# Performance work log

Measured on AMD Instinct MI355X. Metric: run time of the kernel, lower is better.

Reference implementation:

```python
import jax, jax.numpy as jnp
import numpy as np

N, OBS_LEN, PRED_LEN = 8192, 20, 30
EMBED, HIDDEN, CNN_OUT = 64, 128, 2048


def setup_inputs() -> dict:
    key = jax.random.key(0)
    ks = jax.random.split(key, 13)
    s = 0.05
    return {
        "img_embedding": jax.random.normal(ks[0], (N, CNN_OUT), jnp.float32),
        "obs_pos": jax.random.normal(ks[1], (N, OBS_LEN, 2), jnp.float32),
        "obs_hist_size": jax.random.randint(ks[2], (N,), 0, 20, jnp.int64) if jax.config.jax_enable_x64 else jax.random.randint(ks[2], (N,), 0, 20, jnp.int32),
        "obs_pos_rel": jax.random.normal(ks[3], (N, OBS_LEN, 2), jnp.float32),
        "h0": jax.random.normal(ks[4], (1, HIDDEN), jnp.float32) * s,
        "W_ih": jax.random.normal(ks[5], (4 * HIDDEN, EMBED), jnp.float32) * s,
        "W_hh": jax.random.normal(ks[6], (4 * HIDDEN, HIDDEN), jnp.float32) * s,
        "b_ih": jax.random.normal(ks[7], (4 * HIDDEN,), jnp.float32) * s,
        "b_hh": jax.random.normal(ks[8], (4 * HIDDEN,), jnp.float32) * s,
        "embed_W": jax.random.normal(ks[9], (EMBED, 2), jnp.float32) * s,
        "embed_b": jax.random.normal(ks[10], (EMBED,), jnp.float32) * s,
        "pred_W": jax.random.normal(ks[11], (2, HIDDEN + CNN_OUT), jnp.float32) * s,
        "pred_b": jax.random.normal(ks[12], (2,), jnp.float32) * s,
    }


def reference(img_embedding, obs_pos, obs_hist_size, obs_pos_rel,
              h0, W_ih, W_hh, b_ih, b_hh, embed_W, embed_b, pred_W, pred_b):
    n, obs_len = obs_pos.shape[0], obs_pos.shape[1]

    def lstm_cell(x_emb, h, c):
        # torch gate order: i, f, g, o
        gates = x_emb @ W_ih.T + b_ih + h @ W_hh.T + b_hh  # [n, 4H]
        i, f, g, o = jnp.split(gates, 4, axis=-1)
        c2 = jax.nn.sigmoid(f) * c + jax.nn.sigmoid(i) * jnp.tanh(g)
        h2 = jax.nn.sigmoid(o) * jnp.tanh(c2)
        return h2, c2

    def embed(rel):
        return jax.nn.relu(rel @ embed_W.T + embed_b)

    # NOTE: original code initializes BOTH h and c from h0 (faithful to source).
    h = jnp.broadcast_to(h0, (n, h0.shape[1]))
    c = h

    # ---- observation phase: t = 1 .. obs_len-1, masked update ----
    def obs_step(carry, inp):
        h, c = carry
        rel_t, t = inp
        mask = (obs_hist_size > (obs_len - t))[:, None]  # [n, 1]
        h2, c2 = lstm_cell(embed(rel_t), h, c)
        h = jnp.where(mask, h2, h)
        c = jnp.where(mask, c2, c)
        return (h, c), None

    ts = jnp.arange(1, obs_len)
    rel_seq = jnp.swapaxes(obs_pos_rel[:, 1:, :], 0, 1)  # [obs_len-1, n, 2]
    (h, c), _ = jax.lax.scan(obs_step, (h, c), (rel_seq, ts))

    def pred_step(carry, _):
        h, c, pos = carry
        disp = jnp.concatenate([h, img_embedding], axis=1) @ pred_W.T + pred_b  # [n, 2]
        pos = pos + disp
        h, c = lstm_cell(embed(disp), h, c)
        return (h, c, pos), pos

    pos0 = obs_pos[:, -1, :]
    _, traj = jax.lax.scan(pred_step, (h, c, pos0), None, length=PRED_LEN)
    return jnp.swapaxes(traj, 0, 1)  # [n, pred_len, 2]
```

## Files before the change

kernel.cpp:

```cpp
#include <hip/hip_runtime.h>

#define OBS_LEN 20
#define PRED_LEN 30
#define MBLK 32

typedef __attribute__((ext_vector_type(8))) short bf16x8;
typedef __attribute__((ext_vector_type(4))) float f32x4;

__device__ __forceinline__ unsigned short f2bf(float x){
  unsigned int u = __float_as_uint(x);
  u = u + 0x7FFFu + ((u >> 16) & 1u);
  return (unsigned short)(u >> 16);
}

__device__ __forceinline__ float sigm(float x){
  return __builtin_amdgcn_rcpf(1.0f + __expf(-x));
}
__device__ __forceinline__ float tanh_(float x){
  return 1.0f - 2.0f*__builtin_amdgcn_rcpf(__expf(2.0f*x) + 1.0f);
}

__global__ __launch_bounds__(512, 2) void traj_kernel(
    const float* __restrict__ img, const float* __restrict__ obs_pos,
    const int* __restrict__ hist, const float* __restrict__ rel,
    const float* __restrict__ h0, const float* __restrict__ W_ih,
    const float* __restrict__ W_hh, const float* __restrict__ b_ih,
    const float* __restrict__ b_hh, const float* __restrict__ eW,
    const float* __restrict__ eb, const float* __restrict__ pW,
    const float* __restrict__ pb, float* __restrict__ out)
{
  __shared__ unsigned short xh[MBLK*200];
  __shared__ float hf[MBLK*132];
  __shared__ float relL[MBLK*40];
  __shared__ float pwL[2*128];
  __shared__ float eW0[64], eW1[64], ebL[64];
  __shared__ float dispL[MBLK*2];
  __shared__ float imgcL[MBLK*2];

  const int tid  = threadIdx.x;
  const int wv   = tid >> 6;
  const int lane = tid & 63;
  const int q    = lane >> 4;
  const int i    = lane & 15;
  const int j    = wv*16 + i;
  const int g0   = blockIdx.x * MBLK;

  for (int idx = tid; idx < MBLK*40; idx += 512) relL[idx] = rel[g0*40 + idx];
  if (tid < 256) pwL[tid] = pW[(tid >> 7)*2176 + (tid & 127)];
  if (tid < 64){ eW0[tid] = eW[tid*2]; eW1[tid] = eW[tid*2+1]; ebL[tid] = eb[tid]; }

  {
    int m = tid >> 4, i16 = tid & 15;
    const float* row = img + (size_t)(g0 + m)*2048 + i16*128;
    const float* p0  = pW + 128 + i16*128;
    const float* p1  = pW + 2176 + 128 + i16*128;
    float s0 = 0.f, s1 = 0.f;
    #pragma unroll
    for (int v = 0; v < 32; v++){
      float4 a  = ((const float4*)row)[v];
      float4 w0 = ((const float4*)p0)[v];
      float4 w1 = ((const float4*)p1)[v];
      s0 += a.x*w0.x + a.y*w0.y + a.z*w0.z + a.w*w0.w;
      s1 += a.x*w1.x + a.y*w1.y + a.z*w1.z + a.w*w1.w;
    }
    #pragma unroll
    for (int msk = 1; msk < 16; msk <<= 1){
      s0 += __shfl_xor(s0, msk);
      s1 += __shfl_xor(s1, msk);
    }
    if (i16 == 0){ imgcL[m*2] = s0; imgcL[m*2+1] = s1; }
  }

  float h0j = h0[j];
  float bias_s[4];
  #pragma unroll
  for (int nt = 0; nt < 4; nt++) bias_s[nt] = b_ih[nt*128 + j] + b_hh[nt*128 + j];

  int   hist_s[8];
  float c_s[8], h_s[8];
  #pragma unroll
  for (int mt = 0; mt < 2; mt++)
    #pragma unroll
    for (int r = 0; r < 4; r++){
      int m = mt*16 + q*4 + r;
      hist_s[mt*4+r] = hist[g0 + m];
      c_s[mt*4+r] = h0j; h_s[mt*4+r] = h0j;
      xh[m*200 + 64 + j] = f2bf(h0j);
      hf[m*132 + j] = h0j;
    }

  bf16x8 Bf[4][6];
  #pragma unroll
  for (int nt = 0; nt < 4; nt++){
    int row = nt*128 + j;
    #pragma unroll
    for (int kt = 0; kt < 6; kt++){
      const float* src = (kt < 2) ? (W_ih + row*64  + kt*32      + q*8)
                                  : (W_hh + row*128 + (kt-2)*32  + q*8);
      float4 lo = ((const float4*)src)[0];
      float4 hi = ((const float4*)src)[1];
      bf16x8 tf;
      tf[0]=(short)f2bf(lo.x); tf[1]=(short)f2bf(lo.y); tf[2]=(short)f2bf(lo.z); tf[3]=(short)f2bf(lo.w);
      tf[4]=(short)f2bf(hi.x); tf[5]=(short)f2bf(hi.y); tf[6]=(short)f2bf(hi.z); tf[7]=(short)f2bf(hi.w);
      Bf[nt][kt] = tf;
    }
  }

  const int dm  = tid >> 4;
  const int dod = (tid >> 3) & 1;
  float pos_r = obs_pos[(size_t)(g0 + dm)*40 + 38 + dod];
  float pb_r  = pb[dod];
  size_t out_base = (size_t)(g0 + dm)*60 + dod;

  __syncthreads();
  float imgc_r = imgcL[dm*2 + dod];

  f32x4 acc[2][4];

  for (int step = 0; step < 49; step++){
    const bool obs = (step < 19);
    const int  t   = step + 1;
    if (!obs){
      __syncthreads();
      int i8 = tid & 7;
      const float* hrow = &hf[dm*132 + i8*16];
      const float* prow = &pwL[dod*128 + i8*16];
      float s = 0.f;
      #pragma unroll
      for (int v = 0; v < 4; v++){
        float4 h4 = ((const float4*)hrow)[v];
        float4 p4 = ((const float4*)prow)[v];
        s += h4.x*p4.x + h4.y*p4.y + h4.z*p4.z + h4.w*p4.w;
      }
      s += __shfl_xor(s, 1); s += __shfl_xor(s, 2); s += __shfl_xor(s, 4);
      if (i8 == 0){
        float d = s + imgc_r + pb_r;
        pos_r += d;
        out[out_base + (size_t)(step - 19)*2] = pos_r;
        dispL[dm*2 + dod] = d;
      }
    }
    __syncthreads();
    {
      int m  = tid >> 4;
      int e0 = (tid & 15) << 2;
      float r0, r1;
      if (obs){ r0 = relL[m*40 + t*2]; r1 = relL[m*40 + t*2 + 1]; }
      else    { r0 = dispL[m*2];       r1 = dispL[m*2 + 1]; }
      float a0 = fmaxf(0.f, r0*eW0[e0+0] + r1*eW1[e0+0] + ebL[e0+0]);
      float a1 = fmaxf(0.f, r0*eW0[e0+1] + r1*eW1[e0+1] + ebL[e0+1]);
      float a2 = fmaxf(0.f, r0*eW0[e0+2] + r1*eW1[e0+2] + ebL[e0+2]);
      float a3 = fmaxf(0.f, r0*eW0[e0+3] + r1*eW1[e0+3] + ebL[e0+3]);
      unsigned int pk0 = (unsigned int)f2bf(a0) | ((unsigned int)f2bf(a1) << 16);
      unsigned int pk1 = (unsigned int)f2bf(a2) | ((unsigned int)f2bf(a3) << 16);
      *((uint2*)&xh[m*200 + e0]) = make_uint2(pk0, pk1);
    }
    __syncthreads();
    #pragma unroll
    for (int mt = 0; mt < 2; mt++){
      bf16x8 A[6];
      int mrow = mt*16 + i;
      #pragma unroll
      for (int kt = 0; kt < 6; kt++)
        A[kt] = *((const bf16x8*)&xh[mrow*200 + kt*32 + q*8]);
      #pragma unroll
      for (int nt = 0; nt < 4; nt++)
        acc[mt][nt] = (f32x4){bias_s[nt], bias_s[nt], bias_s[nt], bias_s[nt]};
      #pragma unroll
      for (int kt = 0; kt < 6; kt++)
        #pragma unroll
        for (int nt = 0; nt < 4; nt++)
          acc[mt][nt] = __builtin_amdgcn_mfma_f32_16x16x32_bf16(A[kt], Bf[nt][kt], acc[mt][nt], 0, 0, 0);
    }
    __syncthreads();
    #pragma unroll
    for (int mt = 0; mt < 2; mt++)
      #pragma unroll
      for (int r = 0; r < 4; r++){
        int sl = mt*4 + r;
        float ig = acc[mt][0][r];
        float fg = acc[mt][1][r];
        float gg = acc[mt][2][r];
        float og = acc[mt][3][r];
        float c2 = sigm(fg)*c_s[sl] + sigm(ig)*tanh_(gg);
        float h2 = sigm(og)*tanh_(c2);
        if (obs){
          bool upd = hist_s[sl] > (OBS_LEN - t);
          c2 = upd ? c2 : c_s[sl];
          h2 = upd ? h2 : h_s[sl];
        }
        c_s[sl] = c2; h_s[sl] = h2;
        int m = mt*16 + q*4 + r;
        xh[m*200 + 64 + j] = f2bf(h2);
        hf[m*132 + j] = h2;
      }
  }
}

extern "C" void kernel_launch(void* const* d_in, const int* in_sizes, int n_in,
                              void* d_out, int out_size, void* d_ws, size_t ws_size,
                              hipStream_t stream){
  const float* img     = (const float*)d_in[0];
  const float* obs_pos = (const float*)d_in[1];
  const int*   hist    = (const int*)d_in[2];
  const float* rel     = (const float*)d_in[3];
  const float* h0      = (const float*)d_in[4];
  const float* W_ih    = (const float*)d_in[5];
  const float* W_hh    = (const float*)d_in[6];
  const float* b_ih    = (const float*)d_in[7];
  const float* b_hh    = (const float*)d_in[8];
  const float* eW      = (const float*)d_in[9];
  const float* eb      = (const float*)d_in[10];
  const float* pW      = (const float*)d_in[11];
  const float* pb      = (const float*)d_in[12];
  float* out = (float*)d_out;
  hipLaunchKernelGGL(traj_kernel, dim3(8192/MBLK), dim3(512), 0, stream,
                     img, obs_pos, hist, rel, h0, W_ih, W_hh, b_ih, b_hh,
                     eW, eb, pW, pb, out);
}
```

Measured before the change: 268.6 us.

## Double-buffer LSTM input tile and fuse displacement into embedding to cut barriers

The shared xh buffer is split into two ping-pong halves, so the next step's hidden state and observation embedding are written into the other buffer while the current one is read, and the barrier after the MFMA block goes away. The prediction-head dot product now reads the bf16 hidden state directly, dropping the fp32 hf copy. Each 16-lane group computes both displacement components and builds the embedding from them in registers, which removes the dispL round trip and a barrier. In exchange, the prediction head now uses bf16-rounded h, which slightly changes precision.

```diff
diff --git a/kernel.cpp b/kernel.cpp
--- a/kernel.cpp
+++ b/kernel.cpp
@@ -1,7 +1,5 @@
 #include <hip/hip_runtime.h>
 
-#define OBS_LEN 20
-#define PRED_LEN 30
 #define MBLK 32
 
 typedef __attribute__((ext_vector_type(8))) short bf16x8;
@@ -12,7 +10,9 @@
   u = u + 0x7FFFu + ((u >> 16) & 1u);
   return (unsigned short)(u >> 16);
 }
-
+__device__ __forceinline__ float bf2f(unsigned short s){
+  return __uint_as_float(((unsigned int)s) << 16);
+}
 __device__ __forceinline__ float sigm(float x){
   return __builtin_amdgcn_rcpf(1.0f + __expf(-x));
 }
@@ -29,12 +29,10 @@
     const float* __restrict__ eb, const float* __restrict__ pW,
     const float* __restrict__ pb, float* __restrict__ out)
 {
-  __shared__ unsigned short xh[MBLK*200];
-  __shared__ float hf[MBLK*132];
+  __shared__ unsigned short xh[2][MBLK*200];
   __shared__ float relL[MBLK*40];
-  __shared__ float pwL[2*128];
+  __shared__ float pwL[256];
   __shared__ float eW0[64], eW1[64], ebL[64];
-  __shared__ float dispL[MBLK*2];
   __shared__ float imgcL[MBLK*2];
 
   const int tid  = threadIdx.x;
@@ -85,8 +83,7 @@
       int m = mt*16 + q*4 + r;
       hist_s[mt*4+r] = hist[g0 + m];
       c_s[mt*4+r] = h0j; h_s[mt*4+r] = h0j;
-      xh[m*200 + 64 + j] = f2bf(h0j);
-      hf[m*132 + j] = h0j;
+      xh[0][m*200 + 64 + j] = f2bf(h0j);
     }
 
   bf16x8 Bf[4][6];
@@ -107,72 +104,94 @@
   }
 
   const int dm  = tid >> 4;
-  const int dod = (tid >> 3) & 1;
-  float pos_r = obs_pos[(size_t)(g0 + dm)*40 + 38 + dod];
-  float pb_r  = pb[dod];
-  size_t out_base = (size_t)(g0 + dm)*60 + dod;
+  const int i16 = tid & 15;
+  float pos_r = 0.f;
+  if (i16 < 2) pos_r = obs_pos[(size_t)(g0 + dm)*40 + 38 + i16];
 
   __syncthreads();
-  float imgc_r = imgcL[dm*2 + dod];
-
+
+  const float imgc0 = imgcL[dm*2], imgc1 = imgcL[dm*2+1];
+  const float pb0 = pb[0], pb1 = pb[1];
+
+  {
+    int e0 = i16 << 2;
+    float r0 = relL[dm*40 + 2], r1 = relL[dm*40 + 3];
+    float a0 = fmaxf(0.f, r0*eW0[e0+0] + r1*eW1[e0+0] + ebL[e0+0]);
+    float a1 = fmaxf(0.f, r0*eW0[e0+1] + r1*eW1[e0+1] + ebL[e0+1]);
+    float a2 = fmaxf(0.f, r0*eW0[e0+2] + r1*eW1[e0+2] + ebL[e0+2]);
+    float a3 = fmaxf(0.f, r0*eW0[e0+3] + r1*eW1[e0+3] + ebL[e0+3]);
+    unsigned int pk0 = (unsigned int)f2bf(a0) | ((unsigned int)f2bf(a1) << 16);
+    unsigned int pk1 = (unsigned int)f2bf(a2) | ((unsigned int)f2bf(a3) << 16);
+    *((uint2*)&xh[0][dm*200 + e0]) = make_uint2(pk0, pk1);
+  }
+
+  int b = 0;
   f32x4 acc[2][4];
 
   for (int step = 0; step < 49; step++){
     const bool obs = (step < 19);
-    const int  t   = step + 1;
+    __syncthreads();
+
     if (!obs){
+      bf16x8 hv = *((const bf16x8*)&xh[b][dm*200 + 64 + i16*8]);
+      float s0 = 0.f, s1 = 0.f;
+      #pragma unroll
+      for (int u = 0; u < 8; u++){
+        float hfv = bf2f((unsigned short)hv[u]);
+        s0 += hfv * pwL[i16*8 + u];
+        s1 += hfv * pwL[128 + i16*8 + u];
+      }
+      s0 += __shfl_xor(s0, 1); s1 += __shfl_xor(s1, 1);
+      s0 += __shfl_xor(s0, 2); s1 += __shfl_xor(s1, 2);
+      s0 += __shfl_xor(s0, 4); s1 += __shfl_xor(s1, 4);
+      s0 += __shfl_xor(s0, 8); s1 += __shfl_xor(s1, 8);
+      float d0 = s0 + imgc0 + pb0;
+      float d1 = s1 + imgc1 + pb1;
+      if (i16 < 2){
+        pos_r += (i16 == 0) ? d0 : d1;
+        out[(size_t)(g0 + dm)*60 + (size_t)(step - 19)*2 + i16] = pos_r;
+      }
+      int e0 = i16 << 2;
+      float a0 = fmaxf(0.f, d0*eW0[e0+0] + d1*eW1[e0+0] + ebL[e0+0]);
+      float a1 = fmaxf(0.f, d0*eW0[e0+1] + d1*eW1[e0+1] + ebL[e0+1]);
+      float a2 = fmaxf(0.f, d0*eW0[e0+2] + d1*eW1[e0+2] + ebL[e0+2]);
+      float a3 = fmaxf(0.f, d0*eW0[e0+3] + d1*eW1[e0+3] + ebL[e0+3]);
+      unsigned int pk0 = (unsigned int)f2bf(a0) | ((unsigned int)f2bf(a1) << 16);
+      unsigned int pk1 = (unsigned int)f2bf(a2) | ((unsigned int)f2bf(a3) << 16);
+      *((uint2*)&xh[b][dm*200 + e0]) = make_uint2(pk0, pk1);
       __syncthreads();
-      int i8 = tid & 7;
-      const float* hrow = &hf[dm*132 + i8*16];
-      const float* prow = &pwL[dod*128 + i8*16];
-      float s = 0.f;
-      #pragma unroll
-      for (int v = 0; v < 4; v++){
-        float4 h4 = ((const float4*)hrow)[v];
-        float4 p4 = ((const float4*)prow)[v];
-        s += h4.x*p4.x + h4.y*p4.y + h4.z*p4.z + h4.w*p4.w;
-      }
-      s += __shfl_xor(s, 1); s += __shfl_xor(s, 2); s += __shfl_xor(s, 4);
-      if (i8 == 0){
-        float d = s + imgc_r + pb_r;
-        pos_r += d;
-        out[out_base + (size_t)(step - 19)*2] = pos_r;
-        dispL[dm*2 + dod] = d;
-      }
-    }
-    __syncthreads();
-    {
-      int m  = tid >> 4;
-      int e0 = (tid & 15) << 2;
-      float r0, r1;
-      if (obs){ r0 = relL[m*40 + t*2]; r1 = relL[m*40 + t*2 + 1]; }
-      else    { r0 = dispL[m*2];       r1 = dispL[m*2 + 1]; }
+    }
+
+    #pragma unroll
+    for (int mt = 0; mt < 2; mt++){
+      bf16x8 A[6];
+      int mrow = mt*16 + i;
+      #pragma unroll
+      for (int kt = 0; kt < 6; kt++)
+        A[kt] = *((const bf16x8*)&xh[b][mrow*200 + kt*32 + q*8]);
+      #pragma unroll
+      for (int nt = 0; nt < 4; nt++)
+        acc[mt][nt] = (f32x4){bias_s[nt], bias_s[nt], bias_s[nt], bias_s[nt]};
+      #pragma unroll
+      for (int kt = 0; kt < 6; kt++)
+        #pragma unroll
+        for (int nt = 0; nt < 4; nt++)
+          acc[mt][nt] = __builtin_amdgcn_mfma_f32_16x16x32_bf16(A[kt], Bf[nt][kt], acc[mt][nt], 0, 0, 0);
+    }
+
+    if (obs && step < 18){
+      int tt = step + 2;
+      int e0 = i16 << 2;
+      float r0 = relL[dm*40 + tt*2], r1 = relL[dm*40 + tt*2 + 1];
       float a0 = fmaxf(0.f, r0*eW0[e0+0] + r1*eW1[e0+0] + ebL[e0+0]);
       float a1 = fmaxf(0.f, r0*eW0[e0+1] + r1*eW1[e0+1] + ebL[e0+1]);
       float a2 = fmaxf(0.f, r0*eW0[e0+2] + r1*eW1[e0+2] + ebL[e0+2]);
       float a3 = fmaxf(0.f, r0*eW0[e0+3] + r1*eW1[e0+3] + ebL[e0+3]);
       unsigned int pk0 = (unsigned int)f2bf(a0) | ((unsigned int)f2bf(a1) << 16);
       unsigned int pk1 = (unsigned int)f2bf(a2) | ((unsigned int)f2bf(a3) << 16);
-      *((uint2*)&xh[m*200 + e0]) = make_uint2(pk0, pk1);
-    }
-    __syncthreads();
-    #pragma unroll
-    for (int mt = 0; mt < 2; mt++){
-      bf16x8 A[6];
-      int mrow = mt*16 + i;
-      #pragma unroll
-      for (int kt = 0; kt < 6; kt++)
-        A[kt] = *((const bf16x8*)&xh[mrow*200 + kt*32 + q*8]);
-      #pragma unroll
-      for (int nt = 0; nt < 4; nt++)
-        acc[mt][nt] = (f32x4){bias_s[nt], bias_s[nt], bias_s[nt], bias_s[nt]};
-      #pragma unroll
-      for (int kt = 0; kt < 6; kt++)
-        #pragma unroll
-        for (int nt = 0; nt < 4; nt++)
-          acc[mt][nt] = __builtin_amdgcn_mfma_f32_16x16x32_bf16(A[kt], Bf[nt][kt], acc[mt][nt], 0, 0, 0);
-    }
-    __syncthreads();
+      *((uint2*)&xh[b^1][dm*200 + e0]) = make_uint2(pk0, pk1);
+    }
+
     #pragma unroll
     for (int mt = 0; mt < 2; mt++)
       #pragma unroll
@@ -185,15 +204,16 @@
         float c2 = sigm(fg)*c_s[sl] + sigm(ig)*tanh_(gg);
         float h2 = sigm(og)*tanh_(c2);
         if (obs){
-          bool upd = hist_s[sl] > (OBS_LEN - t);
+          bool upd = hist_s[sl] > (19 - step);
           c2 = upd ? c2 : c_s[sl];
           h2 = upd ? h2 : h_s[sl];
         }
         c_s[sl] = c2; h_s[sl] = h2;
         int m = mt*16 + q*4 + r;
-        xh[m*200 + 64 + j] = f2bf(h2);
-        hf[m*132 + j] = h2;
+        xh[b^1][m*200 + 64 + j] = f2bf(h2);
       }
+
+    b ^= 1;
   }
 }
 
```

Measured after the change: 268.6 us. About the same (-0.0%).
